# Kernel tuning notes

Hardware: AMD Instinct MI355X
Metric: run time of the kernel (lower is better)

Reference implementation:

```python
import jax, jax.numpy as jnp
import numpy as np

N_NODES = 100000
N_EDGES = 1600000
F_IN = 128
HID = 128
N_CLS = 40


def setup_inputs() -> dict:
    key = jax.random.key(0)
    ks = jax.random.split(key, 8)
    x = jax.random.normal(ks[0], (N_NODES, F_IN), dtype=jnp.float32)
    edge_index = jax.random.randint(ks[1], (2, N_EDGES), 0, N_NODES, dtype=jnp.int32)
    s1 = 1.0 / np.sqrt(F_IN)
    s2 = 1.0 / np.sqrt(HID)
    W1 = jax.random.normal(ks[2], (F_IN, HID), dtype=jnp.float32) * s1
    b1 = jnp.zeros((HID,), dtype=jnp.float32)
    W2 = jax.random.normal(ks[3], (HID, HID), dtype=jnp.float32) * s2
    b2 = jnp.zeros((HID,), dtype=jnp.float32)
    Wout = jax.random.normal(ks[4], (HID, N_CLS), dtype=jnp.float32) * s2
    bout = jnp.zeros((N_CLS,), dtype=jnp.float32)
    return {"x": x, "edge_index": edge_index, "W1": W1, "b1": b1,
            "W2": W2, "b2": b2, "Wout": Wout, "bout": bout}


def gcn_conv(x, W, b, src, dst, n_nodes):
    """PyG-style GCNConv: h = D^-1/2 (A + I) D^-1/2 (x W) + b."""
    h = x @ W  # [N, H]
    # degree including self-loop
    deg = jnp.zeros((n_nodes,), dtype=h.dtype).at[dst].add(1.0) + 1.0
    dinv = jax.lax.rsqrt(deg)  # [N]
    coeff = dinv[src] * dinv[dst]  # [E]
    msgs = h[src] * coeff[:, None]  # [E, H] gathered messages
    agg = jnp.zeros_like(h).at[dst].add(msgs)
    # self-loop contribution: norm = dinv[i]^2
    agg = agg + h * (dinv * dinv)[:, None]
    return agg + b


def reference(x, edge_index, W1, b1, W2, b2, Wout, bout):
    src, dst = edge_index[0], edge_index[1]
    n = x.shape[0]
    h = jax.nn.relu(gcn_conv(x, W1, b1, src, dst, n))
    # dropout is identity in eval mode
    h = jax.nn.relu(gcn_conv(h, W2, b2, src, dst, n))
    return h @ Wout + bout
```

## Files before the change

kernel.cpp:

```cpp
#include <hip/hip_runtime.h>
#include <hip/hip_bf16.h>
#include <hip/hip_fp16.h>

#define NNODES 100000
#define NEDGES 1600000
#define FD 128
#define NCLS 40
#define DEGCAP 128
#define NBIN 256
#define BINW2 391
#define CAPB2 8192
#define SUBC 1024
#define SBLK 4096

typedef __attribute__((ext_vector_type(8))) short short8;
typedef __attribute__((ext_vector_type(4))) float floatx4;

__device__ __forceinline__ unsigned short f32_bf16_rn(float f) {
    unsigned u = __builtin_bit_cast(unsigned, f);
    u = u + 0x7fffu + ((u >> 16) & 1u);
    return (unsigned short)(u >> 16);
}
__device__ __forceinline__ float bf16_f32(unsigned short h) {
    unsigned u = ((unsigned)h) << 16;
    return __builtin_bit_cast(float, u);
}
__device__ __forceinline__ float4 h4_to_f4(int2 p) {
    __half2 a = __builtin_bit_cast(__half2, p.x);
    __half2 b = __builtin_bit_cast(__half2, p.y);
    float2 fa = __half22float2(a), fb = __half22float2(b);
    return make_float4(fa.x, fa.y, fb.x, fb.y);
}

__device__ __forceinline__ void pack_one(const float* __restrict__ W, int ncols,
                                         int nt_count, short* __restrict__ out,
                                         int id) {
    int lane = id & 63;
    int nt = (id >> 6) % nt_count;
    int ko = id / (64 * nt_count);
    int col = nt * 16 + (lane & 15);
    int kbase = ko * 32 + (lane >> 4) * 8;
    short* dst = out + (size_t)id * 16;
    #pragma unroll
    for (int j = 0; j < 8; ++j) {
        float v = (col < ncols) ? W[(size_t)(kbase + j) * ncols + col] : 0.f;
        unsigned short h = f32_bf16_rn(v);
        float r = v - bf16_f32(h);
        dst[j] = (short)h;
        dst[8 + j] = (short)f32_bf16_rn(r);
    }
}

__global__ __launch_bounds__(256) void prep(const float* __restrict__ W1,
                                            const float* __restrict__ W2,
                                            const float* __restrict__ Wout,
                                            short* __restrict__ w1pk,
                                            short* __restrict__ w2pk,
                                            short* __restrict__ wopk,
                                            int* __restrict__ cursor) {
    int id = blockIdx.x * blockDim.x + threadIdx.x;
    if (id < 2048) pack_one(W1, FD, 8, w1pk, id);
    else if (id < 4096) pack_one(W2, FD, 8, w2pk, id - 2048);
    else if (id < 4864) pack_one(Wout, NCLS, 3, wopk, id - 4096);
    else if (id < 6912) {
        int c = id - 4864;
        cursor[c] = (c >> 3) * CAPB2 + (c & 7) * SUBC;
    }
}

__global__ __launch_bounds__(256) void scatter_k(const int* __restrict__ src,
                                                 const int* __restrict__ dst,
                                                 int* __restrict__ cursor,
                                                 int* __restrict__ ebin) {
    __shared__ int lh[4][NBIN];
    __shared__ int obase[4][NBIN];
    int t = threadIdx.x, wv = t >> 6;
    int g = blockIdx.x & 7;
    int base = blockIdx.x * SBLK;
    for (int i = t; i < 4 * NBIN; i += 256) ((int*)lh)[i] = 0;
    __syncthreads();
    int pay[16];
    unsigned short binv[16], rankv[16];
    #pragma unroll
    for (int i = 0; i < 16; ++i) {
        int idx = base + t + i * 256;
        int b = 0, r = 0, p = -1;
        if (idx < NEDGES) {
            int d = dst[idx];
            b = d / BINW2;
            p = src[idx] | ((d - b * BINW2) << 17);
            r = atomicAdd(&lh[wv][b], 1);
        }
        pay[i] = p; binv[i] = (unsigned short)b; rankv[i] = (unsigned short)r;
    }
    __syncthreads();
    if (t < NBIN) {
        int c0 = lh[0][t], c1 = lh[1][t], c2 = lh[2][t], c3 = lh[3][t];
        int tot = c0 + c1 + c2 + c3;
        int gb = tot ? atomicAdd(&cursor[t * 8 + g], tot) : 0;
        obase[0][t] = gb;
        obase[1][t] = gb + c0;
        obase[2][t] = gb + c0 + c1;
        obase[3][t] = gb + c0 + c1 + c2;
    }
    __syncthreads();
    #pragma unroll
    for (int i = 0; i < 16; ++i) {
        if (pay[i] != -1) {
            int b = binv[i];
            int pos = obase[wv][b] + rankv[i];
            if (pos < b * CAPB2 + (g + 1) * SUBC)
                ebin[pos] = pay[i];
        }
    }
}

__global__ __launch_bounds__(256) void build_bin(const int* __restrict__ ebin,
                                                 const int* __restrict__ cursor,
                                                 int* __restrict__ adj,
                                                 int* __restrict__ rowptr,
                                                 int* __restrict__ degA,
                                                 float* __restrict__ dinv) {
    __shared__ int stage[CAPB2];
    __shared__ int hist[BINW2 + 1];
    __shared__ int rp[BINW2 + 1];
    int bin = blockIdx.x, t = threadIdx.x;
    int off = 0;
    #pragma unroll
    for (int x = 0; x < 8; ++x) {
        int sb = bin * CAPB2 + x * SUBC;
        int nex = cursor[bin * 8 + x] - sb;
        if (nex > SUBC) nex = SUBC;
        for (int i = t; i < nex; i += 256) stage[off + i] = ebin[sb + i];
        off += nex;
    }
    int ne = off;
    for (int i = t; i < BINW2 + 1; i += 256) hist[i] = 0;
    __syncthreads();
    for (int i = t; i < ne; i += 256) atomicAdd(&hist[stage[i] >> 17], 1);
    __syncthreads();
    if (t < 64) {
        int c[7]; int s = 0;
        #pragma unroll
        for (int k = 0; k < 7; ++k) {
            int idx = t * 7 + k;
            c[k] = (idx < BINW2) ? hist[idx] : 0;
            s += c[k];
        }
        int inc = s;
        #pragma unroll
        for (int o = 1; o < 64; o <<= 1) {
            int v = __shfl_up(inc, o);
            if (t >= o) inc += v;
        }
        int excl = inc - s;
        #pragma unroll
        for (int k = 0; k < 7; ++k) {
            int idx = t * 7 + k;
            if (idx < BINW2) { rp[idx] = excl; excl += c[k]; }
        }
    }
    __syncthreads();
    int nbase = bin * BINW2;
    for (int l = t; l < BINW2; l += 256) {
        int node = nbase + l;
        if (node < NNODES) {
            rowptr[node] = bin * CAPB2 + rp[l];
            int dg = hist[l];
            degA[node] = dg;
            dinv[node] = rsqrtf((float)dg + 1.0f);
        }
    }
    __syncthreads();
    for (int i = t; i < BINW2 + 1; i += 256) hist[i] = 0;
    __syncthreads();
    for (int i = t; i < ne; i += 256) {
        int p = stage[i];
        int loc = p >> 17;
        int r = atomicAdd(&hist[loc], 1);
        adj[bin * CAPB2 + rp[loc] + r] = p & 0x1FFFF;
    }
}

__global__ __launch_bounds__(256) void gemm_mfma128_h(const float* __restrict__ X,
                                                      const short* __restrict__ Bpk,
                                                      __half* __restrict__ Y) {
    int w = threadIdx.x >> 6, lane = threadIdx.x & 63;
    int quad = lane >> 4, m = lane & 15;
    int row0 = blockIdx.x * 64 + w * 16;
    int arow = row0 + m;
    bool aok = arow < NNODES;
    floatx4 acc[8];
    #pragma unroll
    for (int nt = 0; nt < 8; ++nt) acc[nt] = (floatx4){0.f, 0.f, 0.f, 0.f};
    #pragma unroll
    for (int ko = 0; ko < 4; ++ko) {
        int kbase = ko * 32 + quad * 8;
        float4 a0 = aok ? *(const float4*)(X + (size_t)arow * FD + kbase)
                        : make_float4(0.f, 0.f, 0.f, 0.f);
        float4 a1 = aok ? *(const float4*)(X + (size_t)arow * FD + kbase + 4)
                        : make_float4(0.f, 0.f, 0.f, 0.f);
        float f[8] = {a0.x, a0.y, a0.z, a0.w, a1.x, a1.y, a1.z, a1.w};
        short8 ahi, alo;
        #pragma unroll
        for (int j = 0; j < 8; ++j) {
            unsigned short h = f32_bf16_rn(f[j]);
            ahi[j] = (short)h;
            alo[j] = (short)f32_bf16_rn(f[j] - bf16_f32(h));
        }
        const short* bp = Bpk + (size_t)(ko * 8) * 64 * 16 + (size_t)lane * 16;
        #pragma unroll
        for (int nt = 0; nt < 8; ++nt) {
            short8 bhi = *(const short8*)bp;
            short8 blo = *(const short8*)(bp + 8);
            bp += 64 * 16;
            acc[nt] = __builtin_amdgcn_mfma_f32_16x16x32_bf16(ahi, bhi, acc[nt], 0, 0, 0);
            acc[nt] = __builtin_amdgcn_mfma_f32_16x16x32_bf16(ahi, blo, acc[nt], 0, 0, 0);
            acc[nt] = __builtin_amdgcn_mfma_f32_16x16x32_bf16(alo, bhi, acc[nt], 0, 0, 0);
        }
    }
    #pragma unroll
    for (int r = 0; r < 4; ++r) {
        int rr = row0 + quad * 4 + r;
        if (rr < NNODES) {
            __half* y = Y + (size_t)rr * FD + m;
            #pragma unroll
            for (int nt = 0; nt < 8; ++nt) y[nt * 16] = __float2half(acc[nt][r]);
        }
    }
}

__global__ __launch_bounds__(256) void gemm_mfma128_hh(const __half* __restrict__ X,
                                                       const short* __restrict__ Bpk,
                                                       __half* __restrict__ Y) {
    int w = threadIdx.x >> 6, lane = threadIdx.x & 63;
    int quad = lane >> 4, m = lane & 15;
    int row0 = blockIdx.x * 64 + w * 16;
    int arow = row0 + m;
    bool aok = arow < NNODES;
    floatx4 acc[8];
    #pragma unroll
    for (int nt = 0; nt < 8; ++nt) acc[nt] = (floatx4){0.f, 0.f, 0.f, 0.f};
    #pragma unroll
    for (int ko = 0; ko < 4; ++ko) {
        int kbase = ko * 32 + quad * 8;
        int4 ar = aok ? *(const int4*)(X + (size_t)arow * FD + kbase)
                      : make_int4(0, 0, 0, 0);
        float4 fa = h4_to_f4(make_int2(ar.x, ar.y));
        float4 fb = h4_to_f4(make_int2(ar.z, ar.w));
        float f[8] = {fa.x, fa.y, fa.z, fa.w, fb.x, fb.y, fb.z, fb.w};
        short8 ahi, alo;
        #pragma unroll
        for (int j = 0; j < 8; ++j) {
            unsigned short h = f32_bf16_rn(f[j]);
            ahi[j] = (short)h;
            alo[j] = (short)f32_bf16_rn(f[j] - bf16_f32(h));
        }
        const short* bp = Bpk + (size_t)(ko * 8) * 64 * 16 + (size_t)lane * 16;
        #pragma unroll
        for (int nt = 0; nt < 8; ++nt) {
            short8 bhi = *(const short8*)bp;
            short8 blo = *(const short8*)(bp + 8);
            bp += 64 * 16;
            acc[nt] = __builtin_amdgcn_mfma_f32_16x16x32_bf16(ahi, bhi, acc[nt], 0, 0, 0);
            acc[nt] = __builtin_amdgcn_mfma_f32_16x16x32_bf16(ahi, blo, acc[nt], 0, 0, 0);
            acc[nt] = __builtin_amdgcn_mfma_f32_16x16x32_bf16(alo, bhi, acc[nt], 0, 0, 0);
        }
    }
    #pragma unroll
    for (int r = 0; r < 4; ++r) {
        int rr = row0 + quad * 4 + r;
        if (rr < NNODES) {
            __half* y = Y + (size_t)rr * FD + m;
            #pragma unroll
            for (int nt = 0; nt < 8; ++nt) y[nt * 16] = __float2half(acc[nt][r]);
        }
    }
}

__global__ __launch_bounds__(256) void gemm_out_mfma_h(const __half* __restrict__ X,
                                                       const short* __restrict__ Bpk,
                                                       const float* __restrict__ bout,
                                                       float* __restrict__ Y) {
    int w = threadIdx.x >> 6, lane = threadIdx.x & 63;
    int quad = lane >> 4, m = lane & 15;
    int row0 = blockIdx.x * 64 + w * 16;
    int arow = row0 + m;
    bool aok = arow < NNODES;
    floatx4 acc[3];
    #pragma unroll
    for (int nt = 0; nt < 3; ++nt) acc[nt] = (floatx4){0.f, 0.f, 0.f, 0.f};
    #pragma unroll
    for (int ko = 0; ko < 4; ++ko) {
        int kbase = ko * 32 + quad * 8;
        int4 ar = aok ? *(const int4*)(X + (size_t)arow * FD + kbase)
                      : make_int4(0, 0, 0, 0);
        float4 fa = h4_to_f4(make_int2(ar.x, ar.y));
        float4 fb = h4_to_f4(make_int2(ar.z, ar.w));
        float f[8] = {fa.x, fa.y, fa.z, fa.w, fb.x, fb.y, fb.z, fb.w};
        short8 ahi, alo;
        #pragma unroll
        for (int j = 0; j < 8; ++j) {
            unsigned short h = f32_bf16_rn(f[j]);
            ahi[j] = (short)h;
            alo[j] = (short)f32_bf16_rn(f[j] - bf16_f32(h));
        }
        const short* bp = Bpk + (size_t)(ko * 3) * 64 * 16 + (size_t)lane * 16;
        #pragma unroll
        for (int nt = 0; nt < 3; ++nt) {
            short8 bhi = *(const short8*)bp;
            short8 blo = *(const short8*)(bp + 8);
            bp += 64 * 16;
            acc[nt] = __builtin_amdgcn_mfma_f32_16x16x32_bf16(ahi, bhi, acc[nt], 0, 0, 0);
            acc[nt] = __builtin_amdgcn_mfma_f32_16x16x32_bf16(ahi, blo, acc[nt], 0, 0, 0);
            acc[nt] = __builtin_amdgcn_mfma_f32_16x16x32_bf16(alo, bhi, acc[nt], 0, 0, 0);
        }
    }
    #pragma unroll
    for (int r = 0; r < 4; ++r) {
        int rr = row0 + quad * 4 + r;
        if (rr < NNODES) {
            #pragma unroll
            for (int nt = 0; nt < 3; ++nt) {
                int col = nt * 16 + m;
                if (col < NCLS)
                    Y[(size_t)rr * NCLS + col] = acc[nt][r] + bout[col];
            }
        }
    }
}

__global__ __launch_bounds__(128) void aggregate_h(const int2* __restrict__ XW2,
                                                   const int* __restrict__ rowptr,
                                                   const int* __restrict__ degA,
                                                   const int* __restrict__ adj,
                                                   const float* __restrict__ dinv,
                                                   const float* __restrict__ bias,
                                                   int2* __restrict__ Yh) {
    __shared__ int ssrc[4][DEGCAP];
    __shared__ float scoef[4][DEGCAP];
    int sub  = threadIdx.x >> 5;
    int lane = threadIdx.x & 31;
    int node = blockIdx.x * 4 + sub;
    float di = dinv[node];
    int deg = degA[node];
    if (deg > DEGCAP) deg = DEGCAP;
    int base = rowptr[node];
    for (int j = lane; j < deg; j += 32) {
        int s = adj[base + j];
        ssrc[sub][j] = s;
        scoef[sub][j] = dinv[s] * di;
    }
    __syncthreads();
    float4 b = *(const float4*)(bias + 4 * lane);
    float4 v = h4_to_f4(XW2[(size_t)node * 32 + lane]);
    float sd = di * di;
    float4 acc;
    acc.x = v.x * sd; acc.y = v.y * sd; acc.z = v.z * sd; acc.w = v.w * sd;
    int j = 0;
    for (; j + 7 < deg; j += 8) {
        int2 p[8];
        float c[8];
        #pragma unroll
        for (int q = 0; q < 8; ++q) {
            p[q] = XW2[(size_t)ssrc[sub][j + q] * 32 + lane];
            c[q] = scoef[sub][j + q];
        }
        #pragma unroll
        for (int q = 0; q < 8; ++q) {
            float4 vq = h4_to_f4(p[q]);
            acc.x = fmaf(vq.x, c[q], acc.x); acc.y = fmaf(vq.y, c[q], acc.y);
            acc.z = fmaf(vq.z, c[q], acc.z); acc.w = fmaf(vq.w, c[q], acc.w);
        }
    }
    for (; j < deg; ++j) {
        float4 v0 = h4_to_f4(XW2[(size_t)ssrc[sub][j] * 32 + lane]);
        float c0 = scoef[sub][j];
        acc.x = fmaf(v0.x, c0, acc.x); acc.y = fmaf(v0.y, c0, acc.y);
        acc.z = fmaf(v0.z, c0, acc.z); acc.w = fmaf(v0.w, c0, acc.w);
    }
    __half2 h01 = __floats2half2_rn(fmaxf(acc.x + b.x, 0.f), fmaxf(acc.y + b.y, 0.f));
    __half2 h23 = __floats2half2_rn(fmaxf(acc.z + b.z, 0.f), fmaxf(acc.w + b.w, 0.f));
    Yh[(size_t)node * 32 + lane] = make_int2(__builtin_bit_cast(int, h01),
                                             __builtin_bit_cast(int, h23));
}

extern "C" void kernel_launch(void* const* d_in, const int* in_sizes, int n_in,
                              void* d_out, int out_size, void* d_ws, size_t ws_size,
                              hipStream_t stream) {
    const float* x    = (const float*)d_in[0];
    const int*   ei   = (const int*)d_in[1];
    const float* W1   = (const float*)d_in[2];
    const float* b1   = (const float*)d_in[3];
    const float* W2   = (const float*)d_in[4];
    const float* b2   = (const float*)d_in[5];
    const float* Wout = (const float*)d_in[6];
    const float* bout = (const float*)d_in[7];
    float* out = (float*)d_out;

    const int* srcv = ei;
    const int* dstv = ei + NEDGES;

    float* bufA   = (float*)d_ws;
    float* bufB   = bufA + (size_t)NNODES * FD;
    int*   adj    = (int*)(bufB + (size_t)NNODES * FD);
    int*   rowptr = adj + (size_t)NBIN * CAPB2;
    int*   degA   = rowptr + NNODES;
    float* dinv   = (float*)(degA + NNODES);
    short* w1pk   = (short*)(dinv + NNODES);
    short* w2pk   = w1pk + 2048 * 16;
    short* wopk   = w2pk + 2048 * 16;
    int*   cursor = (int*)(wopk + 768 * 16);
    int*   ebin   = (int*)bufA;
    __half* xwh   = (__half*)bufA;
    __half* acth  = (__half*)bufB;

    prep<<<27, 256, 0, stream>>>(W1, W2, Wout, w1pk, w2pk, wopk, cursor);

    scatter_k<<<(NEDGES + SBLK - 1) / SBLK, 256, 0, stream>>>(srcv, dstv, cursor, ebin);
    build_bin<<<NBIN, 256, 0, stream>>>(ebin, cursor, adj, rowptr, degA, dinv);

    const int gblocks = (NNODES + 63) / 64;
    gemm_mfma128_h<<<gblocks, 256, 0, stream>>>(x, w1pk, xwh);
    aggregate_h<<<NNODES / 4, 128, 0, stream>>>((const int2*)xwh, rowptr, degA,
                                                adj, dinv, b1, (int2*)acth);
    gemm_mfma128_hh<<<gblocks, 256, 0, stream>>>(acth, w2pk, xwh);
    aggregate_h<<<NNODES / 4, 128, 0, stream>>>((const int2*)xwh, rowptr, degA,
                                                adj, dinv, b2, (int2*)acth);
    gemm_out_mfma_h<<<gblocks, 256, 0, stream>>>(acth, wopk, bout, out);
}
```

Before: 335.6 us.

## Store hidden features in 16-column planes and aggregate per plane

The GEMM outputs are now written in a column-chunked layout (8 planes of 16 halves per node). Each aggregation block handles one plane for 64 nodes, with 4 threads per node reading 32 bytes per neighbour. The intent is that each gather pass touches only a 3.2 MB plane, so it stays resident in cache and random neighbour reads hit cache more often. In exchange, the adjacency list and coefficients are re-read 8 times, the shared-memory staging is dropped, and the DEGCAP clamp is removed.

```diff
diff --git a/kernel.cpp b/kernel.cpp
--- a/kernel.cpp
+++ b/kernel.cpp
@@ -6,7 +6,6 @@
 #define NEDGES 1600000
 #define FD 128
 #define NCLS 40
-#define DEGCAP 128
 #define NBIN 256
 #define BINW2 391
 #define CAPB2 8192
@@ -223,9 +222,9 @@
     for (int r = 0; r < 4; ++r) {
         int rr = row0 + quad * 4 + r;
         if (rr < NNODES) {
-            __half* y = Y + (size_t)rr * FD + m;
             #pragma unroll
-            for (int nt = 0; nt < 8; ++nt) y[nt * 16] = __float2half(acc[nt][r]);
+            for (int nt = 0; nt < 8; ++nt)
+                Y[((size_t)nt * NNODES + rr) * 16 + m] = __float2half(acc[nt][r]);
         }
     }
 }
@@ -244,8 +243,8 @@
     #pragma unroll
     for (int ko = 0; ko < 4; ++ko) {
         int kbase = ko * 32 + quad * 8;
-        int4 ar = aok ? *(const int4*)(X + (size_t)arow * FD + kbase)
-                      : make_int4(0, 0, 0, 0);
+        const __half* ap = X + ((size_t)(kbase >> 4) * NNODES + arow) * 16 + (kbase & 15);
+        int4 ar = aok ? *(const int4*)ap : make_int4(0, 0, 0, 0);
         float4 fa = h4_to_f4(make_int2(ar.x, ar.y));
         float4 fb = h4_to_f4(make_int2(ar.z, ar.w));
         float f[8] = {fa.x, fa.y, fa.z, fa.w, fb.x, fb.y, fb.z, fb.w};
@@ -271,9 +270,9 @@
     for (int r = 0; r < 4; ++r) {
         int rr = row0 + quad * 4 + r;
         if (rr < NNODES) {
-            __half* y = Y + (size_t)rr * FD + m;
             #pragma unroll
-            for (int nt = 0; nt < 8; ++nt) y[nt * 16] = __float2half(acc[nt][r]);
+            for (int nt = 0; nt < 8; ++nt)
+                Y[((size_t)nt * NNODES + rr) * 16 + m] = __float2half(acc[nt][r]);
         }
     }
 }
@@ -293,8 +292,8 @@
     #pragma unroll
     for (int ko = 0; ko < 4; ++ko) {
         int kbase = ko * 32 + quad * 8;
-        int4 ar = aok ? *(const int4*)(X + (size_t)arow * FD + kbase)
-                      : make_int4(0, 0, 0, 0);
+        const __half* ap = X + ((size_t)(kbase >> 4) * NNODES + arow) * 16 + (kbase & 15);
+        int4 ar = aok ? *(const int4*)ap : make_int4(0, 0, 0, 0);
         float4 fa = h4_to_f4(make_int2(ar.x, ar.y));
         float4 fb = h4_to_f4(make_int2(ar.z, ar.w));
         float f[8] = {fa.x, fa.y, fa.z, fa.w, fb.x, fb.y, fb.z, fb.w};
@@ -330,59 +329,62 @@
     }
 }
 
-__global__ __launch_bounds__(128) void aggregate_h(const int2* __restrict__ XW2,
+__global__ __launch_bounds__(256) void aggregate_c(const int2* __restrict__ XWc,
                                                    const int* __restrict__ rowptr,
                                                    const int* __restrict__ degA,
                                                    const int* __restrict__ adj,
                                                    const float* __restrict__ dinv,
                                                    const float* __restrict__ bias,
-                                                   int2* __restrict__ Yh) {
-    __shared__ int ssrc[4][DEGCAP];
-    __shared__ float scoef[4][DEGCAP];
-    int sub  = threadIdx.x >> 5;
-    int lane = threadIdx.x & 31;
-    int node = blockIdx.x * 4 + sub;
+                                                   int2* __restrict__ Yc) {
+    int c = blockIdx.x & 7;
+    int tile = blockIdx.x >> 3;
+    int t = threadIdx.x;
+    int node = tile * 64 + (t >> 2);
+    int q = t & 3;
+    if (node >= NNODES) return;
+    const int2* plane = XWc + (size_t)c * (NNODES * 4);
     float di = dinv[node];
     int deg = degA[node];
-    if (deg > DEGCAP) deg = DEGCAP;
     int base = rowptr[node];
-    for (int j = lane; j < deg; j += 32) {
-        int s = adj[base + j];
-        ssrc[sub][j] = s;
-        scoef[sub][j] = dinv[s] * di;
-    }
-    __syncthreads();
-    float4 b = *(const float4*)(bias + 4 * lane);
-    float4 v = h4_to_f4(XW2[(size_t)node * 32 + lane]);
+    float4 bb = *(const float4*)(bias + c * 16 + q * 4);
+    float4 v = h4_to_f4(plane[(size_t)node * 4 + q]);
     float sd = di * di;
-    float4 acc;
-    acc.x = v.x * sd; acc.y = v.y * sd; acc.z = v.z * sd; acc.w = v.w * sd;
+    float4 acc = make_float4(v.x * sd, v.y * sd, v.z * sd, v.w * sd);
     int j = 0;
     for (; j + 7 < deg; j += 8) {
-        int2 p[8];
-        float c[8];
-        #pragma unroll
-        for (int q = 0; q < 8; ++q) {
-            p[q] = XW2[(size_t)ssrc[sub][j + q] * 32 + lane];
-            c[q] = scoef[sub][j + q];
-        }
-        #pragma unroll
-        for (int q = 0; q < 8; ++q) {
-            float4 vq = h4_to_f4(p[q]);
-            acc.x = fmaf(vq.x, c[q], acc.x); acc.y = fmaf(vq.y, c[q], acc.y);
-            acc.z = fmaf(vq.z, c[q], acc.z); acc.w = fmaf(vq.w, c[q], acc.w);
+        int s[8]; float cf[8]; int2 p[8];
+        #pragma unroll
+        for (int u = 0; u < 8; ++u)
+            s[u] = __builtin_nontemporal_load(adj + base + j + u);
+        #pragma unroll
+        for (int u = 0; u < 8; ++u) {
+            p[u] = plane[(size_t)s[u] * 4 + q];
+            cf[u] = dinv[s[u]] * di;
+        }
+        #pragma unroll
+        for (int u = 0; u < 8; ++u) {
+            float4 vv = h4_to_f4(p[u]);
+            acc.x = fmaf(vv.x, cf[u], acc.x);
+            acc.y = fmaf(vv.y, cf[u], acc.y);
+            acc.z = fmaf(vv.z, cf[u], acc.z);
+            acc.w = fmaf(vv.w, cf[u], acc.w);
         }
     }
     for (; j < deg; ++j) {
-        float4 v0 = h4_to_f4(XW2[(size_t)ssrc[sub][j] * 32 + lane]);
-        float c0 = scoef[sub][j];
-        acc.x = fmaf(v0.x, c0, acc.x); acc.y = fmaf(v0.y, c0, acc.y);
-        acc.z = fmaf(v0.z, c0, acc.z); acc.w = fmaf(v0.w, c0, acc.w);
-    }
-    __half2 h01 = __floats2half2_rn(fmaxf(acc.x + b.x, 0.f), fmaxf(acc.y + b.y, 0.f));
-    __half2 h23 = __floats2half2_rn(fmaxf(acc.z + b.z, 0.f), fmaxf(acc.w + b.w, 0.f));
-    Yh[(size_t)node * 32 + lane] = make_int2(__builtin_bit_cast(int, h01),
-                                             __builtin_bit_cast(int, h23));
+        int s0 = __builtin_nontemporal_load(adj + base + j);
+        float c0 = dinv[s0] * di;
+        float4 vv = h4_to_f4(plane[(size_t)s0 * 4 + q]);
+        acc.x = fmaf(vv.x, c0, acc.x);
+        acc.y = fmaf(vv.y, c0, acc.y);
+        acc.z = fmaf(vv.z, c0, acc.z);
+        acc.w = fmaf(vv.w, c0, acc.w);
+    }
+    __half2 h01 = __floats2half2_rn(fmaxf(acc.x + bb.x, 0.f), fmaxf(acc.y + bb.y, 0.f));
+    __half2 h23 = __floats2half2_rn(fmaxf(acc.z + bb.z, 0.f), fmaxf(acc.w + bb.w, 0.f));
+    long long pv = (long long)(unsigned)__builtin_bit_cast(int, h01)
+                 | ((long long)(unsigned)__builtin_bit_cast(int, h23) << 32);
+    __builtin_nontemporal_store(pv,
+        (long long*)(Yc + (size_t)c * (NNODES * 4) + (size_t)node * 4 + q));
 }
 
 extern "C" void kernel_launch(void* const* d_in, const int* in_sizes, int n_in,
@@ -421,11 +423,12 @@
     build_bin<<<NBIN, 256, 0, stream>>>(ebin, cursor, adj, rowptr, degA, dinv);
 
     const int gblocks = (NNODES + 63) / 64;
+    const int atiles = (NNODES + 63) / 64;
     gemm_mfma128_h<<<gblocks, 256, 0, stream>>>(x, w1pk, xwh);
-    aggregate_h<<<NNODES / 4, 128, 0, stream>>>((const int2*)xwh, rowptr, degA,
+    aggregate_c<<<atiles * 8, 256, 0, stream>>>((const int2*)xwh, rowptr, degA,
                                                 adj, dinv, b1, (int2*)acth);
     gemm_mfma128_hh<<<gblocks, 256, 0, stream>>>(acth, w2pk, xwh);
-    aggregate_h<<<NNODES / 4, 128, 0, stream>>>((const int2*)xwh, rowptr, degA,
+    aggregate_c<<<atiles * 8, 256, 0, stream>>>((const int2*)xwh, rowptr, degA,
                                                 adj, dinv, b2, (int2*)acth);
     gemm_out_mfma_h<<<gblocks, 256, 0, stream>>>(acth, wopk, bout, out);
 }
```

After: 619.4 us. +84.6%, slower.

## Fold source-side dinv into GEMM epilogue and stage weights in LDS

Applied to the files above, without the earlier changes.

The symmetric normalization is split so that each GEMM scales its output row by dinv[row]. Aggregation then becomes a plain sum of gathered rows followed by a single multiply by dinv[dst]. This removes the per-edge coefficient gather (dinv[s]) and the per-edge FMA coefficient from the aggregation, which is the memory-latency-bound hot loop. Separately, each GEMM block first copies the packed weight matrix into shared memory before the MFMA loop. That adds up to 64KB of LDS per block, which may reduce occupancy, and it quantizes the pre-scaled values to fp16.

```diff
diff --git a/kernel.cpp b/kernel.cpp
--- a/kernel.cpp
+++ b/kernel.cpp
@@ -184,7 +184,15 @@
 
 __global__ __launch_bounds__(256) void gemm_mfma128_h(const float* __restrict__ X,
                                                       const short* __restrict__ Bpk,
+                                                      const float* __restrict__ dinv,
                                                       __half* __restrict__ Y) {
+    __shared__ short bs[2048 * 16];
+    {
+        const int4* s = (const int4*)Bpk;
+        int4* d = (int4*)bs;
+        for (int i = threadIdx.x; i < 4096; i += 256) d[i] = s[i];
+    }
+    __syncthreads();
     int w = threadIdx.x >> 6, lane = threadIdx.x & 63;
     int quad = lane >> 4, m = lane & 15;
     int row0 = blockIdx.x * 64 + w * 16;
@@ -208,7 +216,7 @@
             ahi[j] = (short)h;
             alo[j] = (short)f32_bf16_rn(f[j] - bf16_f32(h));
         }
-        const short* bp = Bpk + (size_t)(ko * 8) * 64 * 16 + (size_t)lane * 16;
+        const short* bp = bs + (size_t)(ko * 8) * 64 * 16 + (size_t)lane * 16;
         #pragma unroll
         for (int nt = 0; nt < 8; ++nt) {
             short8 bhi = *(const short8*)bp;
@@ -223,16 +231,25 @@
     for (int r = 0; r < 4; ++r) {
         int rr = row0 + quad * 4 + r;
         if (rr < NNODES) {
+            float sc = dinv[rr];
             __half* y = Y + (size_t)rr * FD + m;
             #pragma unroll
-            for (int nt = 0; nt < 8; ++nt) y[nt * 16] = __float2half(acc[nt][r]);
+            for (int nt = 0; nt < 8; ++nt) y[nt * 16] = __float2half(acc[nt][r] * sc);
         }
     }
 }
 
 __global__ __launch_bounds__(256) void gemm_mfma128_hh(const __half* __restrict__ X,
                                                        const short* __restrict__ Bpk,
+                                                       const float* __restrict__ dinv,
                                                        __half* __restrict__ Y) {
+    __shared__ short bs[2048 * 16];
+    {
+        const int4* s = (const int4*)Bpk;
+        int4* d = (int4*)bs;
+        for (int i = threadIdx.x; i < 4096; i += 256) d[i] = s[i];
+    }
+    __syncthreads();
     int w = threadIdx.x >> 6, lane = threadIdx.x & 63;
     int quad = lane >> 4, m = lane & 15;
     int row0 = blockIdx.x * 64 + w * 16;
@@ -256,7 +273,7 @@
             ahi[j] = (short)h;
             alo[j] = (short)f32_bf16_rn(f[j] - bf16_f32(h));
         }
-        const short* bp = Bpk + (size_t)(ko * 8) * 64 * 16 + (size_t)lane * 16;
+        const short* bp = bs + (size_t)(ko * 8) * 64 * 16 + (size_t)lane * 16;
         #pragma unroll
         for (int nt = 0; nt < 8; ++nt) {
             short8 bhi = *(const short8*)bp;
@@ -271,9 +288,10 @@
     for (int r = 0; r < 4; ++r) {
         int rr = row0 + quad * 4 + r;
         if (rr < NNODES) {
+            float sc = dinv[rr];
             __half* y = Y + (size_t)rr * FD + m;
             #pragma unroll
-            for (int nt = 0; nt < 8; ++nt) y[nt * 16] = __float2half(acc[nt][r]);
+            for (int nt = 0; nt < 8; ++nt) y[nt * 16] = __float2half(acc[nt][r] * sc);
         }
     }
 }
@@ -282,6 +300,13 @@
                                                        const short* __restrict__ Bpk,
                                                        const float* __restrict__ bout,
                                                        float* __restrict__ Y) {
+    __shared__ short bs[768 * 16];
+    {
+        const int4* s = (const int4*)Bpk;
+        int4* d = (int4*)bs;
+        for (int i = threadIdx.x; i < 1536; i += 256) d[i] = s[i];
+    }
+    __syncthreads();
     int w = threadIdx.x >> 6, lane = threadIdx.x & 63;
     int quad = lane >> 4, m = lane & 15;
     int row0 = blockIdx.x * 64 + w * 16;
@@ -305,7 +330,7 @@
             ahi[j] = (short)h;
             alo[j] = (short)f32_bf16_rn(f[j] - bf16_f32(h));
         }
-        const short* bp = Bpk + (size_t)(ko * 3) * 64 * 16 + (size_t)lane * 16;
+        const short* bp = bs + (size_t)(ko * 3) * 64 * 16 + (size_t)lane * 16;
         #pragma unroll
         for (int nt = 0; nt < 3; ++nt) {
             short8 bhi = *(const short8*)bp;
@@ -330,15 +355,14 @@
     }
 }
 
-__global__ __launch_bounds__(128) void aggregate_h(const int2* __restrict__ XW2,
-                                                   const int* __restrict__ rowptr,
-                                                   const int* __restrict__ degA,
-                                                   const int* __restrict__ adj,
-                                                   const float* __restrict__ dinv,
-                                                   const float* __restrict__ bias,
-                                                   int2* __restrict__ Yh) {
+__global__ __launch_bounds__(128) void aggregate_h2(const int2* __restrict__ XW2,
+                                                    const int* __restrict__ rowptr,
+                                                    const int* __restrict__ degA,
+                                                    const int* __restrict__ adj,
+                                                    const float* __restrict__ dinv,
+                                                    const float* __restrict__ bias,
+                                                    int2* __restrict__ Yh) {
     __shared__ int ssrc[4][DEGCAP];
-    __shared__ float scoef[4][DEGCAP];
     int sub  = threadIdx.x >> 5;
     int lane = threadIdx.x & 31;
     int node = blockIdx.x * 4 + sub;
@@ -346,41 +370,31 @@
     int deg = degA[node];
     if (deg > DEGCAP) deg = DEGCAP;
     int base = rowptr[node];
-    for (int j = lane; j < deg; j += 32) {
-        int s = adj[base + j];
-        ssrc[sub][j] = s;
-        scoef[sub][j] = dinv[s] * di;
-    }
+    for (int j = lane; j < deg; j += 32)
+        ssrc[sub][j] = adj[base + j];
     __syncthreads();
     float4 b = *(const float4*)(bias + 4 * lane);
-    float4 v = h4_to_f4(XW2[(size_t)node * 32 + lane]);
-    float sd = di * di;
-    float4 acc;
-    acc.x = v.x * sd; acc.y = v.y * sd; acc.z = v.z * sd; acc.w = v.w * sd;
+    float4 acc = h4_to_f4(XW2[(size_t)node * 32 + lane]);
     int j = 0;
     for (; j + 7 < deg; j += 8) {
         int2 p[8];
-        float c[8];
-        #pragma unroll
-        for (int q = 0; q < 8; ++q) {
+        #pragma unroll
+        for (int q = 0; q < 8; ++q)
             p[q] = XW2[(size_t)ssrc[sub][j + q] * 32 + lane];
-            c[q] = scoef[sub][j + q];
-        }
         #pragma unroll
         for (int q = 0; q < 8; ++q) {
             float4 vq = h4_to_f4(p[q]);
-            acc.x = fmaf(vq.x, c[q], acc.x); acc.y = fmaf(vq.y, c[q], acc.y);
-            acc.z = fmaf(vq.z, c[q], acc.z); acc.w = fmaf(vq.w, c[q], acc.w);
+            acc.x += vq.x; acc.y += vq.y; acc.z += vq.z; acc.w += vq.w;
         }
     }
     for (; j < deg; ++j) {
         float4 v0 = h4_to_f4(XW2[(size_t)ssrc[sub][j] * 32 + lane]);
-        float c0 = scoef[sub][j];
-        acc.x = fmaf(v0.x, c0, acc.x); acc.y = fmaf(v0.y, c0, acc.y);
-        acc.z = fmaf(v0.z, c0, acc.z); acc.w = fmaf(v0.w, c0, acc.w);
-    }
-    __half2 h01 = __floats2half2_rn(fmaxf(acc.x + b.x, 0.f), fmaxf(acc.y + b.y, 0.f));
-    __half2 h23 = __floats2half2_rn(fmaxf(acc.z + b.z, 0.f), fmaxf(acc.w + b.w, 0.f));
+        acc.x += v0.x; acc.y += v0.y; acc.z += v0.z; acc.w += v0.w;
+    }
+    __half2 h01 = __floats2half2_rn(fmaxf(fmaf(acc.x, di, b.x), 0.f),
+                                    fmaxf(fmaf(acc.y, di, b.y), 0.f));
+    __half2 h23 = __floats2half2_rn(fmaxf(fmaf(acc.z, di, b.z), 0.f),
+                                    fmaxf(fmaf(acc.w, di, b.w), 0.f));
     Yh[(size_t)node * 32 + lane] = make_int2(__builtin_bit_cast(int, h01),
                                              __builtin_bit_cast(int, h23));
 }
@@ -421,11 +435,11 @@
     build_bin<<<NBIN, 256, 0, stream>>>(ebin, cursor, adj, rowptr, degA, dinv);
 
     const int gblocks = (NNODES + 63) / 64;
-    gemm_mfma128_h<<<gblocks, 256, 0, stream>>>(x, w1pk, xwh);
-    aggregate_h<<<NNODES / 4, 128, 0, stream>>>((const int2*)xwh, rowptr, degA,
-                                                adj, dinv, b1, (int2*)acth);
-    gemm_mfma128_hh<<<gblocks, 256, 0, stream>>>(acth, w2pk, xwh);
-    aggregate_h<<<NNODES / 4, 128, 0, stream>>>((const int2*)xwh, rowptr, degA,
-                                                adj, dinv, b2, (int2*)acth);
+    gemm_mfma128_h<<<gblocks, 256, 0, stream>>>(x, w1pk, dinv, xwh);
+    aggregate_h2<<<NNODES / 4, 128, 0, stream>>>((const int2*)xwh, rowptr, degA,
+                                                 adj, dinv, b1, (int2*)acth);
+    gemm_mfma128_hh<<<gblocks, 256, 0, stream>>>(acth, w2pk, dinv, xwh);
+    aggregate_h2<<<NNODES / 4, 128, 0, stream>>>((const int2*)xwh, rowptr, degA,
+                                                 adj, dinv, b2, (int2*)acth);
     gemm_out_mfma_h<<<gblocks, 256, 0, stream>>>(acth, wopk, bout, out);
 }
```

Result: no change. 340.2 us (+1.4%).
